# Optimization experiments

Measured on AMD Instinct MI355X. Metric: run time of the kernel, lower is better.

Reference implementation:

```python
import jax, jax.numpy as jnp
import numpy as np

# Static configuration matching the selected code path:
#   mode='inject_subject', is_self_attn=True, layer_id='up_blocks.0' (inject layer, bank hit)
#   alpha = AlphaScheduler.alpha(step=20, total=50, 'up_blocks.0') = 0.8 * 0.6 = 0.48
B, L, D, H = 4, 1024, 1280, 20
DH = D // H  # 64
ALPHA = 0.48


def setup_inputs() -> dict:
    key = jax.random.key(0)
    ks = jax.random.split(key, 8)
    w = lambda k, shp: (jax.random.normal(k, shp, dtype=jnp.float32) * 0.02)
    return {
        "hidden_states": jax.random.normal(ks[0], (B, L, D), dtype=jnp.float32),
        "Wq": w(ks[1], (D, D)),
        "Wk": w(ks[2], (D, D)),
        "Wv": w(ks[3], (D, D)),
        "Wo": w(ks[4], (D, D)),
        "bo": jnp.zeros((D,), dtype=jnp.float32),
        # cached background K/V, stored after head_to_batch_dim -> [B*H, L_bg, DH]
        "K_bg": jax.random.normal(ks[5], (B * H, L, DH), dtype=jnp.float32),
        "V_bg": jax.random.normal(ks[6], (B * H, L, DH), dtype=jnp.float32),
    }


def _head_to_batch(x):  # [B, L, D] -> [B*H, L, DH]
    b, l, _ = x.shape
    return x.reshape(b, l, H, DH).transpose(0, 2, 1, 3).reshape(b * H, l, DH)


def _batch_to_head(x):  # [B*H, L, DH] -> [B, L, D]
    bh, l, _ = x.shape
    b = bh // H
    return x.reshape(b, H, l, DH).transpose(0, 2, 1, 3).reshape(b, l, D)


def reference(hidden_states, Wq, Wk, Wv, Wo, bo, K_bg, V_bg):
    # q/k/v projections (self-attention: k, v from hidden_states)
    q = _head_to_batch(hidden_states @ Wq)  # [B*H, L, DH]
    k = _head_to_batch(hidden_states @ Wk)
    v = _head_to_batch(hidden_states @ Wv)

    # inject_subject: concat cached background K/V scaled by alpha along kv-seq dim
    k = jnp.concatenate([k, ALPHA * K_bg], axis=1)  # [B*H, 2L, DH]
    v = jnp.concatenate([v, ALPHA * V_bg], axis=1)

    # _sdpa: q scaled by scale*sqrt(dh), SDPA divides by sqrt(dh) -> net factor `scale`
    scale = 1.0 / jnp.sqrt(jnp.asarray(DH, dtype=q.dtype))
    scores = jnp.einsum('bqd,bkd->bqk', q, k) * scale  # [B*H, L, 2L]
    probs = jax.nn.softmax(scores, axis=-1)
    context = jnp.einsum('bqk,bkd->bqd', probs, v)  # [B*H, L, DH]

    out = _batch_to_head(context) @ Wo + bo  # to_out[0] linear
    return out
```

## Files before the change

### kernel.cpp

```cpp
#include <hip/hip_runtime.h>
#include <hip/hip_bf16.h>

#define B_   4
#define L_   1024
#define D_   1280
#define H_   20
#define DH_  64
#define BH_  (B_*H_)
#define L2_  (2*L_)
#define ALPHA_ 0.48f
#define QSCALE_ 0.180336880f

typedef __attribute__((ext_vector_type(8))) short short8;
typedef __attribute__((ext_vector_type(4))) float float4v;

__device__ __forceinline__ float exp2_fast(float x) {
    float r;
    asm volatile("v_exp_f32 %0, %1" : "=v"(r) : "v"(x));
    return r;
}

__device__ __forceinline__ ushort f2bf(float f) {
    union { float f; unsigned int i; } v; v.f = f;
    unsigned int i = v.i;
    unsigned int r = i + 0x7FFF + ((i >> 16) & 1);
    return (ushort)(r >> 16);
}
__device__ __forceinline__ short8 pack8(float4 f0, float4 f1) {
    short8 o;
    o[0] = (short)f2bf(f0.x); o[1] = (short)f2bf(f0.y);
    o[2] = (short)f2bf(f0.z); o[3] = (short)f2bf(f0.w);
    o[4] = (short)f2bf(f1.x); o[5] = (short)f2bf(f1.y);
    o[6] = (short)f2bf(f1.z); o[7] = (short)f2bf(f1.w);
    return o;
}
__device__ __forceinline__ void pack4_store(ushort* dst, float a, float b, float c, float d) {
    union { __hip_bfloat162 h; unsigned int u; } x, y;
    x.h = __float22bfloat162_rn(make_float2(a, b));
    y.h = __float22bfloat162_rn(make_float2(c, d));
    uint2 v; v.x = x.u; v.y = y.u;
    *(uint2*)dst = v;
}

__device__ __forceinline__ void async16(const void* g, void* l) {
    __builtin_amdgcn_global_load_lds(
        (__attribute__((address_space(1))) void*)g,
        (__attribute__((address_space(3))) void*)l, 16, 0, 0);
}

__global__ __launch_bounds__(256) void prep(
    const float* __restrict__ w0, const float* __restrict__ w1,
    const float* __restrict__ w2, const float* __restrict__ w3,
    ushort* __restrict__ Wt,
    const float* __restrict__ Vbg, ushort* __restrict__ Vt,
    const float* __restrict__ X, ushort* __restrict__ Xb,
    const float* __restrict__ Kbg, ushort* __restrict__ Kcv) {
    int bi = blockIdx.x, tid = threadIdx.x;
    if (bi < 2880) {
        bool doScale = (bi >= 1600);
        const float* src; ushort* dst; int srcld, dstld; long sbase, dbase;
        if (bi < 1600) {
            int z = bi / 400, t4 = bi % 400;
            int by = t4 / 20, bx = t4 % 20;
            const float* srcs[4] = {w0, w1, w2, w3};
            src = srcs[z]; srcld = D_; dstld = D_;
            sbase = (long)(by * 64) * D_ + bx * 64;
            dst = Wt + (long)z * D_ * D_;
            dbase = (long)(bx * 64) * D_ + by * 64;
        } else {
            int j = bi - 1600;
            int bh = j >> 4, kt = j & 15;
            src = Vbg; srcld = DH_; dstld = L2_;
            sbase = ((long)bh * L_ + kt * 64) * DH_;
            dst = Vt;
            dbase = (long)bh * DH_ * L2_ + L_ + kt * 64;
        }
        __shared__ ushort t[64 * 72];
        int ldr = tid >> 3, ldc = (tid & 7) * 8;
#pragma unroll
        for (int i = 0; i < 2; i++) {
            int y = ldr + 32 * i;
            long idx = sbase + (long)y * srcld + ldc;
            float4 f0 = *(const float4*)&src[idx];
            float4 f1 = *(const float4*)&src[idx + 4];
            if (doScale) {
                f0.x *= ALPHA_; f0.y *= ALPHA_; f0.z *= ALPHA_; f0.w *= ALPHA_;
                f1.x *= ALPHA_; f1.y *= ALPHA_; f1.z *= ALPHA_; f1.w *= ALPHA_;
            }
            *(short8*)&t[y * 72 + ldc] = pack8(f0, f1);
        }
        __syncthreads();
        int r8 = (tid & 7) * 8, c0 = tid >> 3;
#pragma unroll
        for (int i = 0; i < 2; i++) {
            int c = c0 + i * 32;
            short8 o;
#pragma unroll
            for (int j2 = 0; j2 < 8; j2++) o[j2] = (short)t[(r8 + j2) * 72 + c];
            *(short8*)&dst[dbase + (long)c * dstld + r8] = o;
        }
    } else if (bi < 5440) {
        long i = ((long)(bi - 2880) * 256 + tid) * 8;
        *(short8*)&Xb[i] = pack8(*(const float4*)&X[i], *(const float4*)&X[i + 4]);
    } else {
        long i = ((long)(bi - 5440) * 256 + tid) * 8;
        *(short8*)&Kcv[i] = pack8(*(const float4*)&Kbg[i], *(const float4*)&Kbg[i + 4]);
    }
}

template<int BMt, int BNt, int WROWS, int WCOLS>
__global__ __launch_bounds__(256) void gemm_tpl(
    const ushort* __restrict__ A, const ushort* __restrict__ Bt,
    ushort* __restrict__ Qp, ushort* __restrict__ Kp, ushort* __restrict__ Vt,
    float* __restrict__ Out, const float* __restrict__ bo, int mode) {
    constexpr int MI = BMt / WROWS / 16;
    constexpr int NI = BNt / WCOLS / 16;
    constexpr int ASZ = BMt * 32, BSZ = BNt * 32;
    constexpr int RB = 1280 / BNt;
    __shared__ __align__(16) ushort Al[2 * ASZ];
    __shared__ __align__(16) ushort Bl[2 * BSZ];
    int tid = threadIdx.x;
    int bx = blockIdx.x, by = blockIdx.y;
    int w = tid >> 6, lane = tid & 63, l15 = lane & 15, quad = lane >> 4;
    int wm = (w / WCOLS) * (BMt / WROWS);
    int wn = (w % WCOLS) * (BNt / WCOLS);
    float4v acc[MI][NI] = {};
    const int K = 1280;
    constexpr int NK = 40;
    const ushort* Arow = A + (long)by * BMt * K + (tid >> 2) * K + (tid & 3) * 8;
    const ushort* Brow = Bt + (long)bx * BNt * K + (tid >> 2) * K + (tid & 3) * 8;

    auto stage = [&](int ki, int b) {
#pragma unroll
        for (int i = 0; i < BMt / 64; i++)
            async16(Arow + (long)i * 64 * K + ki * 32, &Al[b * ASZ + (i * 4 + w) * 512]);
#pragma unroll
        for (int i = 0; i < BNt / 64; i++)
            async16(Brow + (long)i * 64 * K + ki * 32, &Bl[b * BSZ + (i * 4 + w) * 512]);
    };

    stage(0, 0);
    __syncthreads();
    for (int ki = 0; ki < NK; ki++) {
        int cur = ki & 1;
        if (ki + 1 < NK) stage(ki + 1, 1 - cur);
        short8 av[MI], bv[NI];
#pragma unroll
        for (int mi = 0; mi < MI; mi++)
            av[mi] = *(const short8*)&Al[cur * ASZ + (wm + mi * 16 + l15) * 32 + quad * 8];
#pragma unroll
        for (int ni = 0; ni < NI; ni++)
            bv[ni] = *(const short8*)&Bl[cur * BSZ + (wn + ni * 16 + l15) * 32 + quad * 8];
#pragma unroll
        for (int mi = 0; mi < MI; mi++)
#pragma unroll
            for (int ni = 0; ni < NI; ni++)
                acc[mi][ni] = __builtin_amdgcn_mfma_f32_16x16x32_bf16(av[mi], bv[ni], acc[mi][ni], 0, 0, 0);
        __syncthreads();
    }

    if (mode == 0) {
        int which = bx / RB;
#pragma unroll
        for (int mi = 0; mi < MI; mi++) {
            int m0 = by * BMt + wm + mi * 16 + quad * 4;
            int b = m0 >> 10, l0 = m0 & 1023;
#pragma unroll
            for (int ni = 0; ni < NI; ni++) {
                int n = bx * BNt + wn + ni * 16 + l15;
                int np = n - which * 1280;
                int h = np >> 6, dh = np & 63;
                if (which == 0) {
#pragma unroll
                    for (int r = 0; r < 4; r++)
                        Qp[((long)(b * H_ + h) * L_ + l0 + r) * DH_ + dh] =
                            f2bf(acc[mi][ni][r] * QSCALE_);
                } else if (which == 1) {
#pragma unroll
                    for (int r = 0; r < 4; r++)
                        Kp[((long)(b * H_ + h) * L_ + l0 + r) * DH_ + dh] =
                            f2bf(acc[mi][ni][r]);
                } else {
                    pack4_store(&Vt[((long)(b * H_ + h) * DH_ + dh) * L2_ + l0],
                                acc[mi][ni][0], acc[mi][ni][1],
                                acc[mi][ni][2], acc[mi][ni][3]);
                }
            }
        }
    } else {
#pragma unroll
        for (int mi = 0; mi < MI; mi++) {
            int mloc = wm + mi * 16 + quad * 4;
#pragma unroll
            for (int ni = 0; ni < NI; ni++) {
                int nloc = wn + ni * 16 + l15;
#pragma unroll
                for (int r = 0; r < 4; r++) {
                    int m = by * BMt + mloc + r;
                    int n = bx * BNt + nloc;
                    Out[(long)m * D_ + n] = acc[mi][ni][r] + bo[n];
                }
            }
        }
    }
}

#define FS 72

__global__ __launch_bounds__(256) void flash_attn(
    const ushort* __restrict__ Qp, const ushort* __restrict__ Kp,
    const ushort* __restrict__ Kbg, const ushort* __restrict__ Vt,
    ushort* __restrict__ Ctx) {
    __shared__ __align__(16) ushort Kl[2 * 4096], Vl[2 * 4096];
    __shared__ __align__(16) ushort Pl[128 * FS];
    int tid = threadIdx.x;
    int w = tid >> 6, lane = tid & 63, l15 = lane & 15, quad = lane >> 4;
    int bi = blockIdx.x;
    int bh = (bi & 7) * 10 + ((bi >> 3) % 10);
    int qt = bi / 80;

    short8 aq[2][2];
    const ushort* Qb = Qp + ((long)bh * L_ + qt * 128 + w * 32) * DH_;
#pragma unroll
    for (int mi = 0; mi < 2; mi++)
#pragma unroll
        for (int ks = 0; ks < 2; ks++)
            aq[mi][ks] = *(const short8*)&Qb[(mi * 16 + l15) * DH_ + ks * 32 + quad * 8];

    float rs[2] = {0.f, 0.f};
    float4v O[2][4] = {};
    const ushort* Vb = Vt + (long)bh * DH_ * L2_;
    int prow = (w * 32 + l15) * FS;

    auto stage = [&](int kt, int b) {
        const ushort* Ksrc = (kt < 16)
            ? Kp  + ((long)bh * L_ + kt * 64) * DH_
            : Kbg + ((long)bh * L_ + (kt - 16) * 64) * DH_;
#pragma unroll
        for (int i = 0; i < 2; i++) {
            int c = w * 2 + i;
            async16(&Ksrc[(long)lane * DH_ + c * 8], &Kl[b * 4096 + c * 512]);
            async16(&Vb[(long)lane * L2_ + kt * 64 + c * 8], &Vl[b * 4096 + c * 512]);
        }
    };

    stage(0, 0);
    __syncthreads();
    for (int kt = 0; kt < 32; kt++) {
        int cur = kt & 1;
        if (kt + 1 < 32) stage(kt + 1, 1 - cur);
        bool bg = (kt >= 16);
        float4v s[4][2] = {};
#pragma unroll
        for (int ks = 0; ks < 2; ks++) {
            short8 bk[4];
#pragma unroll
            for (int nt = 0; nt < 4; nt++)
                bk[nt] = *(const short8*)&Kl[cur * 4096 + (ks * 4 + quad) * 512 + (nt * 16 + l15) * 8];
#pragma unroll
            for (int nt = 0; nt < 4; nt++)
#pragma unroll
                for (int mi = 0; mi < 2; mi++)
                    s[nt][mi] = __builtin_amdgcn_mfma_f32_16x16x32_bf16(bk[nt], aq[mi][ks], s[nt][mi], 0, 0, 0);
        }
#pragma unroll
        for (int nt = 0; nt < 4; nt++)
#pragma unroll
            for (int mi = 0; mi < 2; mi++) {
                float p[4];
#pragma unroll
                for (int r = 0; r < 4; r++) {
                    float sv = s[nt][mi][r];
                    if (bg) sv *= ALPHA_;
                    p[r] = exp2_fast(sv);
                    rs[mi] += p[r];
                }
                pack4_store(&Pl[prow + mi * 16 * FS + nt * 16 + quad * 4],
                            p[0], p[1], p[2], p[3]);
            }
        asm volatile("s_waitcnt lgkmcnt(0)" ::: "memory");
        __builtin_amdgcn_sched_barrier(0);
#pragma unroll
        for (int ks = 0; ks < 2; ks++) {
            short8 bv[4];
#pragma unroll
            for (int nt = 0; nt < 4; nt++)
                bv[nt] = *(const short8*)&Vl[cur * 4096 + (ks * 4 + quad) * 512 + (nt * 16 + l15) * 8];
            short8 ap[2];
#pragma unroll
            for (int mi = 0; mi < 2; mi++)
                ap[mi] = *(const short8*)&Pl[prow + mi * 16 * FS + ks * 32 + quad * 8];
#pragma unroll
            for (int nt = 0; nt < 4; nt++)
#pragma unroll
                for (int mi = 0; mi < 2; mi++)
                    O[mi][nt] = __builtin_amdgcn_mfma_f32_16x16x32_bf16(bv[nt], ap[mi], O[mi][nt], 0, 0, 0);
        }
        __syncthreads();
    }
    int b = bh / H_, h = bh % H_;
#pragma unroll
    for (int mi = 0; mi < 2; mi++) {
        float v = rs[mi];
        v += __shfl_xor(v, 16);
        v += __shfl_xor(v, 32);
        float rcp = 1.f / v;
        long l = qt * 128 + w * 32 + mi * 16 + l15;
#pragma unroll
        for (int nt = 0; nt < 4; nt++)
            pack4_store(&Ctx[(long)(b * L_ + l) * D_ + h * DH_ + nt * 16 + quad * 4],
                        O[mi][nt][0] * rcp, O[mi][nt][1] * rcp,
                        O[mi][nt][2] * rcp, O[mi][nt][3] * rcp);
    }
}

extern "C" void kernel_launch(void* const* d_in, const int* in_sizes, int n_in,
                              void* d_out, int out_size, void* d_ws, size_t ws_size,
                              hipStream_t stream) {
    const float* X   = (const float*)d_in[0];
    const float* Wq  = (const float*)d_in[1];
    const float* Wk  = (const float*)d_in[2];
    const float* Wv  = (const float*)d_in[3];
    const float* Wo  = (const float*)d_in[4];
    const float* bo  = (const float*)d_in[5];
    const float* Kbg = (const float*)d_in[6];
    const float* Vbg = (const float*)d_in[7];

    char* ws = (char*)d_ws;
    size_t off = 0;
    auto alloc = [&](size_t bytes) {
        void* p = ws + off;
        off = (off + bytes + 255) & ~(size_t)255;
        return p;
    };
    ushort* Wt    = (ushort*)alloc((size_t)4 * D_ * D_ * 2);
    ushort* Qp    = (ushort*)alloc((size_t)BH_ * L_ * DH_ * 2);
    ushort* Kp    = (ushort*)alloc((size_t)BH_ * L_ * DH_ * 2);
    ushort* Kcv   = (ushort*)alloc((size_t)BH_ * L_ * DH_ * 2);
    ushort* Vt    = (ushort*)alloc((size_t)BH_ * DH_ * L2_ * 2);
    ushort* Xb    = (ushort*)alloc((size_t)B_ * L_ * D_ * 2);
    ushort* Ctx   = Xb;
    ushort* Wqkv_t = Wt;
    ushort* Wo_t   = Wt + (size_t)3 * D_ * D_;

    prep<<<8000, 256, 0, stream>>>(Wq, Wk, Wv, Wo, Wt, Vbg, Vt, X, Xb, Kbg, Kcv);
    gemm_tpl<128, 128, 2, 2><<<dim3(30, 32), 256, 0, stream>>>(
        Xb, Wqkv_t, Qp, Kp, Vt, nullptr, nullptr, 0);
    flash_attn<<<dim3(640), 256, 0, stream>>>(Qp, Kp, Kcv, Vt, Ctx);
    gemm_tpl<64, 128, 1, 4><<<dim3(10, 64), 256, 0, stream>>>(
        Ctx, Wo_t, nullptr, nullptr, nullptr, (float*)d_out, bo, 1);
}
```

Baseline: 311.8 us.

## Store K and V tiles in pre-swizzled contiguous 64x64 blocks for async LDS loads

Changes the global layout of K (projected and background) and transposed V into per-tile contiguous 8-element chunked blocks that match the LDS layout the attention kernel expects. The attention kernel's global_load_lds calls then read fully contiguous 512-element segments instead of strided rows, improving coalescing. The prep kernel and the QKV GEMM epilogue are rewritten to produce the new layout, and the prep grid shrinks because the Kbg path now processes one 64x64 tile per block. The K epilogue now does scattered 2-byte stores, which may cost more in the GEMM.

```diff
diff --git a/kernel.cpp b/kernel.cpp
--- a/kernel.cpp
+++ b/kernel.cpp
@@ -56,9 +56,12 @@
     const float* __restrict__ X, ushort* __restrict__ Xb,
     const float* __restrict__ Kbg, ushort* __restrict__ Kcv) {
     int bi = blockIdx.x, tid = threadIdx.x;
+    __shared__ __align__(16) ushort t[64 * 72];
     if (bi < 2880) {
         bool doScale = (bi >= 1600);
-        const float* src; ushort* dst; int srcld, dstld; long sbase, dbase;
+        const float* src; int srcld; long sbase;
+        ushort* dst = nullptr; int dstld = 0; long dbase = 0;
+        ushort* vout = nullptr;
         if (bi < 1600) {
             int z = bi / 400, t4 = bi % 400;
             int by = t4 / 20, bx = t4 % 20;
@@ -70,12 +73,10 @@
         } else {
             int j = bi - 1600;
             int bh = j >> 4, kt = j & 15;
-            src = Vbg; srcld = DH_; dstld = L2_;
+            src = Vbg; srcld = DH_;
             sbase = ((long)bh * L_ + kt * 64) * DH_;
-            dst = Vt;
-            dbase = (long)bh * DH_ * L2_ + L_ + kt * 64;
-        }
-        __shared__ ushort t[64 * 72];
+            vout = Vt + (((long)bh * 32 + 16 + kt) << 12);
+        }
         int ldr = tid >> 3, ldc = (tid & 7) * 8;
 #pragma unroll
         for (int i = 0; i < 2; i++) {
@@ -90,21 +91,50 @@
             *(short8*)&t[y * 72 + ldc] = pack8(f0, f1);
         }
         __syncthreads();
-        int r8 = (tid & 7) * 8, c0 = tid >> 3;
-#pragma unroll
-        for (int i = 0; i < 2; i++) {
-            int c = c0 + i * 32;
-            short8 o;
-#pragma unroll
-            for (int j2 = 0; j2 < 8; j2++) o[j2] = (short)t[(r8 + j2) * 72 + c];
-            *(short8*)&dst[dbase + (long)c * dstld + r8] = o;
+        if (bi < 1600) {
+            int r8 = (tid & 7) * 8, c0 = tid >> 3;
+#pragma unroll
+            for (int i = 0; i < 2; i++) {
+                int c = c0 + i * 32;
+                short8 o;
+#pragma unroll
+                for (int j2 = 0; j2 < 8; j2++) o[j2] = (short)t[(r8 + j2) * 72 + c];
+                *(short8*)&dst[dbase + (long)c * dstld + r8] = o;
+            }
+        } else {
+#pragma unroll
+            for (int i = 0; i < 2; i++) {
+                int jj = i * 256 + tid;
+                int cc = jj >> 6, d2 = jj & 63;
+                short8 o;
+#pragma unroll
+                for (int e = 0; e < 8; e++) o[e] = (short)t[(cc * 8 + e) * 72 + d2];
+                *(short8*)&vout[(long)jj * 8] = o;
+            }
         }
     } else if (bi < 5440) {
         long i = ((long)(bi - 2880) * 256 + tid) * 8;
         *(short8*)&Xb[i] = pack8(*(const float4*)&X[i], *(const float4*)&X[i + 4]);
     } else {
-        long i = ((long)(bi - 5440) * 256 + tid) * 8;
-        *(short8*)&Kcv[i] = pack8(*(const float4*)&Kbg[i], *(const float4*)&Kbg[i + 4]);
+        int j2 = bi - 5440;
+        int bh = j2 >> 4, kt = j2 & 15;
+        const float* src = Kbg + ((long)bh * L_ + kt * 64) * DH_;
+#pragma unroll
+        for (int i = 0; i < 2; i++) {
+            int r = i * 256 + tid;
+            int kv = r >> 3, cd = r & 7;
+            long idx = (long)kv * 64 + cd * 8;
+            *(short8*)&t[kv * 72 + cd * 8] =
+                pack8(*(const float4*)&src[idx], *(const float4*)&src[idx + 4]);
+        }
+        __syncthreads();
+        ushort* outp = Kcv + (((long)bh * 16 + kt) << 12);
+#pragma unroll
+        for (int i = 0; i < 2; i++) {
+            int jj = i * 256 + tid;
+            int c = jj >> 6, kv = jj & 63;
+            *(short8*)&outp[(long)jj * 8] = *(const short8*)&t[kv * 72 + c * 8];
+        }
     }
 }
 
@@ -176,12 +206,14 @@
                         Qp[((long)(b * H_ + h) * L_ + l0 + r) * DH_ + dh] =
                             f2bf(acc[mi][ni][r] * QSCALE_);
                 } else if (which == 1) {
+                    long kb = ((((long)(b * H_ + h) * 16 + (l0 >> 6)) * 8 + (dh >> 3)) * 64
+                               + (l0 & 63)) * 8 + (dh & 7);
 #pragma unroll
                     for (int r = 0; r < 4; r++)
-                        Kp[((long)(b * H_ + h) * L_ + l0 + r) * DH_ + dh] =
-                            f2bf(acc[mi][ni][r]);
+                        Kp[kb + r * 8] = f2bf(acc[mi][ni][r]);
                 } else {
-                    pack4_store(&Vt[((long)(b * H_ + h) * DH_ + dh) * L2_ + l0],
+                    pack4_store(&Vt[((((long)(b * H_ + h) * 32 + (l0 >> 6)) * 8
+                                      + ((l0 & 63) >> 3)) * 64 + dh) * 8 + (l0 & 7)],
                                 acc[mi][ni][0], acc[mi][ni][1],
                                 acc[mi][ni][2], acc[mi][ni][3]);
                 }
@@ -229,18 +261,18 @@
 
     float rs[2] = {0.f, 0.f};
     float4v O[2][4] = {};
-    const ushort* Vb = Vt + (long)bh * DH_ * L2_;
     int prow = (w * 32 + l15) * FS;
 
     auto stage = [&](int kt, int b) {
         const ushort* Ksrc = (kt < 16)
-            ? Kp  + ((long)bh * L_ + kt * 64) * DH_
-            : Kbg + ((long)bh * L_ + (kt - 16) * 64) * DH_;
+            ? Kp  + (((long)bh * 16 + kt) << 12)
+            : Kbg + (((long)bh * 16 + (kt - 16)) << 12);
+        const ushort* Vsrc = Vt + (((long)bh * 32 + kt) << 12);
 #pragma unroll
         for (int i = 0; i < 2; i++) {
             int c = w * 2 + i;
-            async16(&Ksrc[(long)lane * DH_ + c * 8], &Kl[b * 4096 + c * 512]);
-            async16(&Vb[(long)lane * L2_ + kt * 64 + c * 8], &Vl[b * 4096 + c * 512]);
+            async16(&Ksrc[c * 512 + lane * 8], &Kl[b * 4096 + c * 512]);
+            async16(&Vsrc[c * 512 + lane * 8], &Vl[b * 4096 + c * 512]);
         }
     };
 
@@ -343,7 +375,7 @@
     ushort* Wqkv_t = Wt;
     ushort* Wo_t   = Wt + (size_t)3 * D_ * D_;
 
-    prep<<<8000, 256, 0, stream>>>(Wq, Wk, Wv, Wo, Wt, Vbg, Vt, X, Xb, Kbg, Kcv);
+    prep<<<6720, 256, 0, stream>>>(Wq, Wk, Wv, Wo, Wt, Vbg, Vt, X, Xb, Kbg, Kcv);
     gemm_tpl<128, 128, 2, 2><<<dim3(30, 32), 256, 0, stream>>>(
         Xb, Wqkv_t, Qp, Kp, Vt, nullptr, nullptr, 0);
     flash_attn<<<dim3(640), 256, 0, stream>>>(Qp, Kp, Kcv, Vt, Ctx);
```

New measurement: 309.2 us. Within noise of the previous version (-0.8%).
